# Kernel tuning notes

Hardware: AMD Instinct MI355X
Metric: run time of the kernel (lower is better)

The kernel has to match this reference:

```python
import jax, jax.numpy as jnp
import numpy as np

DN = ('NCDHW', 'OIDHW', 'NCDHW')  # torch Conv3d layout

def conv3d(x, w, b, pad):
    y = jax.lax.conv_general_dilated(x, w, (1, 1, 1), [(p, p) for p in pad], dimension_numbers=DN)
    return y + b[None, :, None, None, None]

def setup_inputs() -> dict:
    key = jax.random.key(0)
    ks = jax.random.split(key, 10)
    C, Cq = 64, 8  # in_channels, in_channels // 8
    s = 0.05
    x = jax.random.normal(ks[0], (2, C, 16, 16, 16), dtype=jnp.float32)
    return {
        'x': x,
        'wq': jax.random.normal(ks[1], (Cq, C, 1, 3, 1), jnp.float32) * s,
        'bq': jax.random.normal(ks[2], (Cq,), jnp.float32) * s,
        'wk': jax.random.normal(ks[3], (Cq, C, 3, 1, 1), jnp.float32) * s,
        'bk': jax.random.normal(ks[4], (Cq,), jnp.float32) * s,
        'wj': jax.random.normal(ks[5], (Cq, C, 1, 1, 3), jnp.float32) * s,
        'bj': jax.random.normal(ks[6], (Cq,), jnp.float32) * s,
        'wv': jax.random.normal(ks[7], (C, C, 1, 1, 1), jnp.float32) * s,
        'bv': jax.random.normal(ks[8], (C,), jnp.float32) * s,
        'gamma': jax.random.normal(ks[9], (1,), jnp.float32) * s,
    }

def reference(x, wq, bq, wk, bk, wj, bj, wv, bv, gamma):
    B, C, H, W, D = x.shape
    N = H * W * D
    q = conv3d(x, wq, bq, (0, 1, 0)).reshape(B, -1, N)   # [B, c, N]
    k = conv3d(x, wk, bk, (1, 0, 0)).reshape(B, -1, N)   # [B, c, N]
    j = conv3d(x, wj, bj, (0, 0, 1)).reshape(B, -1, N)   # [B, c, N]
    # affinity = (Q^T K) (J^T K) reassociated as Q^T (K J^T) K  -- identical math,
    # O(N^2 c) instead of O(N^3) since c = C//8 << N.
    kj = jnp.einsum('bcn,bdn->bcd', k, j)                # [B, c, c] = K @ J^T
    aff = jnp.einsum('bcn,bcd,bdm->bnm', q, kj, k)       # [B, N, N]
    aff = jax.nn.softmax(aff, axis=-1)
    v = conv3d(x, wv, bv, (0, 0, 0)).reshape(B, C, N)    # [B, C, N]
    weights = jnp.einsum('bcn,bnm->bcm', v, aff).reshape(B, C, H, W, D)
    return gamma * weights + x
```

## Files before the change

### kernel.cpp

```cpp
#include <hip/hip_runtime.h>

#define N 4096
#define CIN 64
#define NB 2

typedef unsigned short u16;
typedef short bf16x8 __attribute__((ext_vector_type(8)));
typedef float f32x4 __attribute__((ext_vector_type(4)));

#define OFF_QT 0
#define OFF_KT (OFF_QT + NB*N*8)
#define OFF_JT (OFF_KT + NB*N*8)
#define OFF_V  (OFF_JT + NB*N*8)
#define OFF_QK (OFF_V + NB*CIN*N)
#define OFF_MX (OFF_QK + NB*N*8)
#define OFF_SC (OFF_MX + NB*N)

__device__ __forceinline__ u16 f2bf(float f) {
    union { float f; unsigned u; } v; v.f = f;
    unsigned r = (v.u + 0x7fffu + ((v.u >> 16) & 1u)) >> 16;
    return (u16)r;
}

__global__ __launch_bounds__(512, 4) void prep(
        const float* __restrict__ x,
        const float* __restrict__ wq, const float* __restrict__ bq,
        const float* __restrict__ wk, const float* __restrict__ bk,
        const float* __restrict__ wj, const float* __restrict__ bj,
        const float* __restrict__ wv, const float* __restrict__ bv,
        float* __restrict__ ws, u16* __restrict__ vbf, float* __restrict__ out) {
    __shared__ union {
        float qkj[3][256];
        float accv[256][8];
    } sh;
    const int t    = threadIdx.x;
    const int tn   = t & 255;
    const int half = t >> 8;
    const int y    = blockIdx.y;
    const int b    = blockIdx.z;
    const int n    = blockIdx.x * 256 + tn;
    const float* xb = x + (size_t)b * CIN * N + n;
    const int c0base = half * 32;

    if (y < 8) {
        int cq = y;
        int d = n & 15, w = (n >> 4) & 15, h = n >> 8;
        int owl = (w > 0) ? -16 : 0,  owh = (w < 15) ? 16 : 0;
        int ohl = (h > 0) ? -256 : 0, ohh = (h < 15) ? 256 : 0;
        int odl = (d > 0) ? -1 : 0,   odh = (d < 15) ? 1 : 0;
        float mwl = (w > 0) ? 1.f : 0.f, mwh = (w < 15) ? 1.f : 0.f;
        float mhl = (h > 0) ? 1.f : 0.f, mhh = (h < 15) ? 1.f : 0.f;
        float mdl = (d > 0) ? 1.f : 0.f, mdh = (d < 15) ? 1.f : 0.f;
        float q = half ? 0.f : bq[cq];
        float k = half ? 0.f : bk[cq];
        float j = half ? 0.f : bj[cq];
        for (int c0i = 0; c0i < 32; c0i += 8) {
            const int c0 = c0base + c0i;
            float xc[8], xwl[8], xwh[8], xhl[8], xhh[8], xdl[8], xdh[8];
#pragma unroll
            for (int u = 0; u < 8; ++u) {
                const float* p = xb + (size_t)(c0 + u) * N;
                xc[u]  = p[0];
                xwl[u] = p[owl]; xwh[u] = p[owh];
                xhl[u] = p[ohl]; xhh[u] = p[ohh];
                xdl[u] = p[odl]; xdh[u] = p[odh];
            }
#pragma unroll
            for (int u = 0; u < 8; ++u) {
                int c = c0 + u;
                const float* wqr = wq + (cq * CIN + c) * 3;
                const float* wkr = wk + (cq * CIN + c) * 3;
                const float* wjr = wj + (cq * CIN + c) * 3;
                q += wqr[0] * (xwl[u] * mwl) + wqr[1] * xc[u] + wqr[2] * (xwh[u] * mwh);
                k += wkr[0] * (xhl[u] * mhl) + wkr[1] * xc[u] + wkr[2] * (xhh[u] * mhh);
                j += wjr[0] * (xdl[u] * mdl) + wjr[1] * xc[u] + wjr[2] * (xdh[u] * mdh);
            }
        }
        if (half) { sh.qkj[0][tn] = q; sh.qkj[1][tn] = k; sh.qkj[2][tn] = j; }
        __syncthreads();
        if (!half) {
            q += sh.qkj[0][tn]; k += sh.qkj[1][tn]; j += sh.qkj[2][tn];
            size_t base = (size_t)(b * N + n) * 8 + cq;
            ws[OFF_QT + base] = q;
            ws[OFF_KT + base] = k;
            ws[OFF_JT + base] = j;
        }
    } else {
        int yy = y - 8;
        int co0 = yy * 8;
        float acc[8];
#pragma unroll
        for (int i = 0; i < 8; ++i) acc[i] = half ? 0.f : bv[co0 + i];
        for (int c0i = 0; c0i < 32; c0i += 8) {
            const int c0 = c0base + c0i;
            float xv[8];
#pragma unroll
            for (int u = 0; u < 8; ++u) xv[u] = xb[(size_t)(c0 + u) * N];
#pragma unroll
            for (int u = 0; u < 8; ++u)
#pragma unroll
                for (int i = 0; i < 8; ++i)
                    acc[i] += wv[(co0 + i) * CIN + c0 + u] * xv[u];
            if ((c0 >> 3) == yy) {
#pragma unroll
                for (int u = 0; u < 8; ++u)
                    out[(size_t)(b * CIN + c0 + u) * N + n] = xv[u];
            }
        }
        if (half) {
#pragma unroll
            for (int i = 0; i < 8; ++i) sh.accv[tn][i] = acc[i];
        }
        __syncthreads();
        if (!half) {
#pragma unroll
            for (int i = 0; i < 8; ++i)
                vbf[(size_t)(b * CIN + co0 + i) * N + n] = f2bf(acc[i] + sh.accv[tn][i]);
        }
    }
}

__global__ __launch_bounds__(256) void kjqkj(const float* __restrict__ ws_in,
                                             float* __restrict__ ws) {
    __shared__ float kjpart[4][64];
    __shared__ float kjs[64];
    const int t = threadIdx.x, lane = t & 63, wid = t >> 6;
    const int b = blockIdx.y;
    const float* ktb = ws_in + OFF_KT + (size_t)b * N * 8;
    const float* jtb = ws_in + OFF_JT + (size_t)b * N * 8;
    const float* qtb = ws_in + OFF_QT + (size_t)b * N * 8;

    float acc[64];
#pragma unroll
    for (int i = 0; i < 64; ++i) acc[i] = 0.f;
    for (int i = 0; i < 16; ++i) {
        int nn = i * 256 + t;
        const float4* kt = (const float4*)(ktb + (size_t)nn * 8);
        const float4* jt = (const float4*)(jtb + (size_t)nn * 8);
        float4 ka = kt[0], kb = kt[1], ja = jt[0], jb = jt[1];
        float kv[8] = {ka.x, ka.y, ka.z, ka.w, kb.x, kb.y, kb.z, kb.w};
        float jv[8] = {ja.x, ja.y, ja.z, ja.w, jb.x, jb.y, jb.z, jb.w};
#pragma unroll
        for (int c = 0; c < 8; ++c)
#pragma unroll
            for (int dd = 0; dd < 8; ++dd) acc[c * 8 + dd] += kv[c] * jv[dd];
    }
#pragma unroll
    for (int s = 32; s >= 1; s >>= 1)
#pragma unroll
        for (int i = 0; i < 64; ++i) acc[i] += __shfl_down(acc[i], s, 64);
    if (lane == 0) {
#pragma unroll
        for (int i = 0; i < 64; ++i) kjpart[wid][i] = acc[i];
    }
    __syncthreads();
    if (t < 64) kjs[t] = kjpart[0][t] + kjpart[1][t] + kjpart[2][t] + kjpart[3][t];
    __syncthreads();

    float kjr[64];
#pragma unroll
    for (int i = 0; i < 64; ++i) kjr[i] = kjs[i];
    int m = blockIdx.x * 256 + t;
    const float4* qt = (const float4*)(qtb + (size_t)m * 8);
    float4 qa = qt[0], qb = qt[1];
    float qv[8] = {qa.x, qa.y, qa.z, qa.w, qb.x, qb.y, qb.z, qb.w};
    float o[8];
#pragma unroll
    for (int dd = 0; dd < 8; ++dd) {
        float a = 0.f;
#pragma unroll
        for (int c = 0; c < 8; ++c) a += qv[c] * kjr[c * 8 + dd];
        o[dd] = a;
    }
    float4* dst = (float4*)(ws + OFF_QK + (size_t)(b * N + m) * 8);
    dst[0] = make_float4(o[0], o[1], o[2], o[3]);
    dst[1] = make_float4(o[4], o[5], o[6], o[7]);
}

__global__ __launch_bounds__(512, 4) void pass1(const float* __restrict__ ws,
                                                float* __restrict__ mx_o, float* __restrict__ sc_o,
                                                const float* __restrict__ gamma) {
    __shared__ float smx[8][4];
    __shared__ float ssum[8][4];
    const int t = threadIdx.x, lane = t & 63, wid = t >> 6;
    const int r0 = blockIdx.x * 4;
    const int b  = r0 >> 12;
    const float* ktb = ws + OFF_KT + (size_t)b * N * 8;

    float4 qa[4], qb[4];
#pragma unroll
    for (int rr = 0; rr < 4; ++rr) {
        const float4* q4 = (const float4*)(ws + OFF_QK + (size_t)(r0 + rr) * 8);
        qa[rr] = q4[0]; qb[rr] = q4[1];
    }

    float as[4][8];
#pragma unroll
    for (int i = 0; i < 8; ++i) {
        const int m = wid * 512 + i * 64 + lane;
        const float4* kk4 = (const float4*)(ktb + (size_t)m * 8);
        float4 ka = kk4[0], kb2 = kk4[1];
#pragma unroll
        for (int rr = 0; rr < 4; ++rr)
            as[rr][i] = qa[rr].x * ka.x + qa[rr].y * ka.y + qa[rr].z * ka.z + qa[rr].w * ka.w
                      + qb[rr].x * kb2.x + qb[rr].y * kb2.y + qb[rr].z * kb2.z + qb[rr].w * kb2.w;
    }

    float mx[4];
#pragma unroll
    for (int rr = 0; rr < 4; ++rr) {
        float m01 = fmaxf(fmaxf(as[rr][0], as[rr][1]), fmaxf(as[rr][2], as[rr][3]));
        float m23 = fmaxf(fmaxf(as[rr][4], as[rr][5]), fmaxf(as[rr][6], as[rr][7]));
        mx[rr] = fmaxf(m01, m23);
    }
#pragma unroll
    for (int s = 32; s >= 1; s >>= 1)
#pragma unroll
        for (int rr = 0; rr < 4; ++rr)
            mx[rr] = fmaxf(mx[rr], __shfl_xor(mx[rr], s, 64));
    if (lane == 0) {
#pragma unroll
        for (int rr = 0; rr < 4; ++rr) smx[wid][rr] = mx[rr];
    }
    __syncthreads();
    float gm[4];
#pragma unroll
    for (int rr = 0; rr < 4; ++rr) {
        float g0 = fmaxf(fmaxf(smx[0][rr], smx[1][rr]), fmaxf(smx[2][rr], smx[3][rr]));
        float g1 = fmaxf(fmaxf(smx[4][rr], smx[5][rr]), fmaxf(smx[6][rr], smx[7][rr]));
        gm[rr] = fmaxf(g0, g1);
    }

    float sm[4];
#pragma unroll
    for (int rr = 0; rr < 4; ++rr) {
        float s0 = __expf(as[rr][0] - gm[rr]) + __expf(as[rr][1] - gm[rr])
                 + __expf(as[rr][2] - gm[rr]) + __expf(as[rr][3] - gm[rr]);
        float s1 = __expf(as[rr][4] - gm[rr]) + __expf(as[rr][5] - gm[rr])
                 + __expf(as[rr][6] - gm[rr]) + __expf(as[rr][7] - gm[rr]);
        sm[rr] = s0 + s1;
    }
#pragma unroll
    for (int s = 32; s >= 1; s >>= 1)
#pragma unroll
        for (int rr = 0; rr < 4; ++rr)
            sm[rr] += __shfl_xor(sm[rr], s, 64);
    if (lane == 0) {
#pragma unroll
        for (int rr = 0; rr < 4; ++rr) ssum[wid][rr] = sm[rr];
    }
    __syncthreads();
    if (t < 4) {
        float g0 = fmaxf(fmaxf(smx[0][t], smx[1][t]), fmaxf(smx[2][t], smx[3][t]));
        float g1 = fmaxf(fmaxf(smx[4][t], smx[5][t]), fmaxf(smx[6][t], smx[7][t]));
        float g  = fmaxf(g0, g1);
        float tt = ((ssum[0][t] + ssum[1][t]) + (ssum[2][t] + ssum[3][t]))
                 + ((ssum[4][t] + ssum[5][t]) + (ssum[6][t] + ssum[7][t]));
        mx_o[r0 + t] = g;
        sc_o[r0 + t] = gamma[0] / tt;
    }
}

__global__ __launch_bounds__(256) void pass2(const float* __restrict__ ws,
                                             const u16* __restrict__ vbf,
                                             float* __restrict__ out) {
    __shared__ u16 Pt[64][72];
    __shared__ u16 Vt[64][72];
    __shared__ float ks[64][8];
    const int t  = threadIdx.x;
    const int b  = blockIdx.z;
    const int m0 = blockIdx.x * 64;
    const int ns = blockIdx.y;
    const float* qkT = ws + OFF_QK + (size_t)b * N * 8;
    const float* ktb = ws + OFF_KT + (size_t)b * N * 8;
    const float* mxv = ws + OFF_MX + (size_t)b * N;
    const float* scv = ws + OFF_SC + (size_t)b * N;
    const u16*   vb  = vbf + (size_t)b * CIN * N;

    if (t < 128) ((float4*)ks)[t] = ((const float4*)(ktb + (size_t)m0 * 8))[t];

    const int lane = t & 63;
    const int wid  = t >> 6;
    const int l16  = lane & 15;
    const int lq   = lane >> 4;
    const int vc   = t >> 3;
    const int vseg = t & 7;

    f32x4 acc[4];
#pragma unroll
    for (int i = 0; i < 4; ++i) acc[i] = (f32x4){0.f, 0.f, 0.f, 0.f};

    for (int ch = 0; ch < 8; ++ch) {
        const int n0 = ns * 512 + ch * 64;
        const int n  = n0 + lane;
        const float4* q4 = (const float4*)(qkT + (size_t)n * 8);
        float4 qa = q4[0], qb = q4[1];
        float mxl = mxv[n], sl = scv[n];
        uint4 v0 = *(const uint4*)(vb + (size_t)vc        * N + n0 + vseg * 8);
        uint4 v1 = *(const uint4*)(vb + (size_t)(vc + 32) * N + n0 + vseg * 8);
        __syncthreads();
#pragma unroll
        for (int r = 0; r < 16; ++r) {
            int mi = wid * 16 + r;
            float4 k0 = *(const float4*)&ks[mi][0];
            float4 k1 = *(const float4*)&ks[mi][4];
            float a = qa.x * k0.x + qa.y * k0.y + qa.z * k0.z + qa.w * k0.w
                    + qb.x * k1.x + qb.y * k1.y + qb.z * k1.z + qb.w * k1.w;
            Pt[mi][lane] = f2bf(__expf(a - mxl) * sl);
        }
        *(uint4*)&Vt[vc][vseg * 8]      = v0;
        *(uint4*)&Vt[vc + 32][vseg * 8] = v1;
        __syncthreads();
#pragma unroll
        for (int kk = 0; kk < 2; ++kk) {
            int k0i = kk * 32 + lq * 8;
            bf16x8 bfrag = *(const bf16x8*)&Pt[wid * 16 + l16][k0i];
#pragma unroll
            for (int ct = 0; ct < 4; ++ct) {
                bf16x8 afrag = *(const bf16x8*)&Vt[ct * 16 + l16][k0i];
                acc[ct] = __builtin_amdgcn_mfma_f32_16x16x32_bf16(afrag, bfrag, acc[ct], 0, 0, 0);
            }
        }
    }
    float* ob = out + (size_t)b * CIN * N;
    const int mcol = m0 + wid * 16 + l16;
#pragma unroll
    for (int ct = 0; ct < 4; ++ct)
#pragma unroll
        for (int r = 0; r < 4; ++r) {
            int c = ct * 16 + lq * 4 + r;
            atomicAdd(&ob[(size_t)c * N + mcol], acc[ct][r]);
        }
}

extern "C" void kernel_launch(void* const* d_in, const int* in_sizes, int n_in,
                              void* d_out, int out_size, void* d_ws, size_t ws_size,
                              hipStream_t stream) {
    const float* x  = (const float*)d_in[0];
    const float* wq = (const float*)d_in[1];
    const float* bq = (const float*)d_in[2];
    const float* wk = (const float*)d_in[3];
    const float* bk = (const float*)d_in[4];
    const float* wj = (const float*)d_in[5];
    const float* bj = (const float*)d_in[6];
    const float* wv = (const float*)d_in[7];
    const float* bv = (const float*)d_in[8];
    const float* gamma = (const float*)d_in[9];
    float* ws  = (float*)d_ws;
    float* out = (float*)d_out;
    u16* vbf = (u16*)(ws + OFF_V);

    prep<<<dim3(16, 16, 2), 512, 0, stream>>>(x, wq, bq, wk, bk, wj, bj, wv, bv, ws, vbf, out);
    kjqkj<<<dim3(16, 2), 256, 0, stream>>>(ws, ws);
    pass1<<<2048, 512, 0, stream>>>(ws, ws + OFF_MX, ws + OFF_SC, gamma);
    pass2<<<dim3(64, 8, 2), 256, 0, stream>>>(ws, vbf, out);
}
```

Before: 155.7 us.

## Fuse KJ reduction into prep and Q·KJ projection into pass1, drop kjqkj kernel

Prep now computes all 8 q/k/j channels in one block per spatial tile instead of one block per channel, and emits partial K·J^T sums per tile into the workspace. Pass1 sums those 16 partials and forms Q·KJ on the fly, so the separate kjqkj launch and its serialized single-block-per-batch reduction are removed. The change also narrows pass2's LDS row padding from 72 to 68. The tradeoffs are higher register pressure in the fused qkj branch, redundant KJ summation in every pass1 block, and possible LDS bank conflicts from the new padding.

```diff
diff --git a/kernel.cpp b/kernel.cpp
--- a/kernel.cpp
+++ b/kernel.cpp
@@ -15,6 +15,7 @@
 #define OFF_QK (OFF_V + NB*CIN*N)
 #define OFF_MX (OFF_QK + NB*N*8)
 #define OFF_SC (OFF_MX + NB*N)
+#define OFF_KJ (OFF_SC + NB*N)
 
 __device__ __forceinline__ u16 f2bf(float f) {
     union { float f; unsigned u; } v; v.f = f;
@@ -30,20 +31,22 @@
         const float* __restrict__ wv, const float* __restrict__ bv,
         float* __restrict__ ws, u16* __restrict__ vbf, float* __restrict__ out) {
     __shared__ union {
-        float qkj[3][256];
+        float qkj[3][8][256];
         float accv[256][8];
     } sh;
+    __shared__ float kjpart[4][64];
     const int t    = threadIdx.x;
     const int tn   = t & 255;
     const int half = t >> 8;
     const int y    = blockIdx.y;
+    const int bx   = blockIdx.x;
     const int b    = blockIdx.z;
-    const int n    = blockIdx.x * 256 + tn;
+    const int n    = bx * 256 + tn;
     const float* xb = x + (size_t)b * CIN * N + n;
     const int c0base = half * 32;
 
-    if (y < 8) {
-        int cq = y;
+    if (y == 8) {
+        const int lane = t & 63, wid = t >> 6;
         int d = n & 15, w = (n >> 4) & 15, h = n >> 8;
         int owl = (w > 0) ? -16 : 0,  owh = (w < 15) ? 16 : 0;
         int ohl = (h > 0) ? -256 : 0, ohh = (h < 15) ? 256 : 0;
@@ -51,9 +54,13 @@
         float mwl = (w > 0) ? 1.f : 0.f, mwh = (w < 15) ? 1.f : 0.f;
         float mhl = (h > 0) ? 1.f : 0.f, mhh = (h < 15) ? 1.f : 0.f;
         float mdl = (d > 0) ? 1.f : 0.f, mdh = (d < 15) ? 1.f : 0.f;
-        float q = half ? 0.f : bq[cq];
-        float k = half ? 0.f : bk[cq];
-        float j = half ? 0.f : bj[cq];
+        float q[8], k[8], j[8];
+#pragma unroll
+        for (int cq = 0; cq < 8; ++cq) {
+            q[cq] = half ? 0.f : bq[cq];
+            k[cq] = half ? 0.f : bk[cq];
+            j[cq] = half ? 0.f : bj[cq];
+        }
         for (int c0i = 0; c0i < 32; c0i += 8) {
             const int c0 = c0base + c0i;
             float xc[8], xwl[8], xwh[8], xhl[8], xhh[8], xdl[8], xdh[8];
@@ -68,25 +75,69 @@
 #pragma unroll
             for (int u = 0; u < 8; ++u) {
                 int c = c0 + u;
-                const float* wqr = wq + (cq * CIN + c) * 3;
-                const float* wkr = wk + (cq * CIN + c) * 3;
-                const float* wjr = wj + (cq * CIN + c) * 3;
-                q += wqr[0] * (xwl[u] * mwl) + wqr[1] * xc[u] + wqr[2] * (xwh[u] * mwh);
-                k += wkr[0] * (xhl[u] * mhl) + wkr[1] * xc[u] + wkr[2] * (xhh[u] * mhh);
-                j += wjr[0] * (xdl[u] * mdl) + wjr[1] * xc[u] + wjr[2] * (xdh[u] * mdh);
-            }
-        }
-        if (half) { sh.qkj[0][tn] = q; sh.qkj[1][tn] = k; sh.qkj[2][tn] = j; }
+                float xwlm = xwl[u] * mwl, xwhm = xwh[u] * mwh;
+                float xhlm = xhl[u] * mhl, xhhm = xhh[u] * mhh;
+                float xdlm = xdl[u] * mdl, xdhm = xdh[u] * mdh;
+                float xcc  = xc[u];
+#pragma unroll
+                for (int cq = 0; cq < 8; ++cq) {
+                    const float* wqr = wq + (cq * CIN + c) * 3;
+                    const float* wkr = wk + (cq * CIN + c) * 3;
+                    const float* wjr = wj + (cq * CIN + c) * 3;
+                    q[cq] += wqr[0] * xwlm + wqr[1] * xcc + wqr[2] * xwhm;
+                    k[cq] += wkr[0] * xhlm + wkr[1] * xcc + wkr[2] * xhhm;
+                    j[cq] += wjr[0] * xdlm + wjr[1] * xcc + wjr[2] * xdhm;
+                }
+            }
+        }
+        if (half) {
+#pragma unroll
+            for (int cq = 0; cq < 8; ++cq) {
+                sh.qkj[0][cq][tn] = q[cq];
+                sh.qkj[1][cq][tn] = k[cq];
+                sh.qkj[2][cq][tn] = j[cq];
+            }
+        }
         __syncthreads();
         if (!half) {
-            q += sh.qkj[0][tn]; k += sh.qkj[1][tn]; j += sh.qkj[2][tn];
-            size_t base = (size_t)(b * N + n) * 8 + cq;
-            ws[OFF_QT + base] = q;
-            ws[OFF_KT + base] = k;
-            ws[OFF_JT + base] = j;
+#pragma unroll
+            for (int cq = 0; cq < 8; ++cq) {
+                q[cq] += sh.qkj[0][cq][tn];
+                k[cq] += sh.qkj[1][cq][tn];
+                j[cq] += sh.qkj[2][cq][tn];
+            }
+            size_t base = (size_t)(b * N + n) * 8;
+#pragma unroll
+            for (int cq = 0; cq < 8; ++cq) {
+                ws[OFF_QT + base + cq] = q[cq];
+                ws[OFF_KT + base + cq] = k[cq];
+                ws[OFF_JT + base + cq] = j[cq];
+            }
+#pragma unroll
+            for (int g = 0; g < 4; ++g) {
+                float a16[16];
+#pragma unroll
+                for (int cc = 0; cc < 2; ++cc)
+#pragma unroll
+                    for (int dd = 0; dd < 8; ++dd)
+                        a16[cc * 8 + dd] = k[g * 2 + cc] * j[dd];
+#pragma unroll
+                for (int s = 32; s >= 1; s >>= 1)
+#pragma unroll
+                    for (int i = 0; i < 16; ++i) a16[i] += __shfl_down(a16[i], s, 64);
+                if (lane == 0) {
+#pragma unroll
+                    for (int i = 0; i < 16; ++i) kjpart[wid][g * 16 + i] = a16[i];
+                }
+            }
+        }
+        __syncthreads();
+        if (t < 64) {
+            float s = kjpart[0][t] + kjpart[1][t] + kjpart[2][t] + kjpart[3][t];
+            ws[OFF_KJ + (size_t)(b * 16 + bx) * 64 + t] = s;
         }
     } else {
-        int yy = y - 8;
+        int yy = y;
         int co0 = yy * 8;
         float acc[8];
 #pragma unroll
@@ -120,78 +171,50 @@
     }
 }
 
-__global__ __launch_bounds__(256) void kjqkj(const float* __restrict__ ws_in,
-                                             float* __restrict__ ws) {
-    __shared__ float kjpart[4][64];
+__global__ __launch_bounds__(512, 4) void pass1(const float* __restrict__ ws_in,
+                                                float* __restrict__ ws,
+                                                const float* __restrict__ gamma) {
     __shared__ float kjs[64];
-    const int t = threadIdx.x, lane = t & 63, wid = t >> 6;
-    const int b = blockIdx.y;
-    const float* ktb = ws_in + OFF_KT + (size_t)b * N * 8;
-    const float* jtb = ws_in + OFF_JT + (size_t)b * N * 8;
-    const float* qtb = ws_in + OFF_QT + (size_t)b * N * 8;
-
-    float acc[64];
-#pragma unroll
-    for (int i = 0; i < 64; ++i) acc[i] = 0.f;
-    for (int i = 0; i < 16; ++i) {
-        int nn = i * 256 + t;
-        const float4* kt = (const float4*)(ktb + (size_t)nn * 8);
-        const float4* jt = (const float4*)(jtb + (size_t)nn * 8);
-        float4 ka = kt[0], kb = kt[1], ja = jt[0], jb = jt[1];
-        float kv[8] = {ka.x, ka.y, ka.z, ka.w, kb.x, kb.y, kb.z, kb.w};
-        float jv[8] = {ja.x, ja.y, ja.z, ja.w, jb.x, jb.y, jb.z, jb.w};
-#pragma unroll
-        for (int c = 0; c < 8; ++c)
-#pragma unroll
-            for (int dd = 0; dd < 8; ++dd) acc[c * 8 + dd] += kv[c] * jv[dd];
-    }
-#pragma unroll
-    for (int s = 32; s >= 1; s >>= 1)
-#pragma unroll
-        for (int i = 0; i < 64; ++i) acc[i] += __shfl_down(acc[i], s, 64);
-    if (lane == 0) {
-#pragma unroll
-        for (int i = 0; i < 64; ++i) kjpart[wid][i] = acc[i];
-    }
-    __syncthreads();
-    if (t < 64) kjs[t] = kjpart[0][t] + kjpart[1][t] + kjpart[2][t] + kjpart[3][t];
-    __syncthreads();
-
-    float kjr[64];
-#pragma unroll
-    for (int i = 0; i < 64; ++i) kjr[i] = kjs[i];
-    int m = blockIdx.x * 256 + t;
-    const float4* qt = (const float4*)(qtb + (size_t)m * 8);
-    float4 qa = qt[0], qb = qt[1];
-    float qv[8] = {qa.x, qa.y, qa.z, qa.w, qb.x, qb.y, qb.z, qb.w};
-    float o[8];
-#pragma unroll
-    for (int dd = 0; dd < 8; ++dd) {
-        float a = 0.f;
-#pragma unroll
-        for (int c = 0; c < 8; ++c) a += qv[c] * kjr[c * 8 + dd];
-        o[dd] = a;
-    }
-    float4* dst = (float4*)(ws + OFF_QK + (size_t)(b * N + m) * 8);
-    dst[0] = make_float4(o[0], o[1], o[2], o[3]);
-    dst[1] = make_float4(o[4], o[5], o[6], o[7]);
-}
-
-__global__ __launch_bounds__(512, 4) void pass1(const float* __restrict__ ws,
-                                                float* __restrict__ mx_o, float* __restrict__ sc_o,
-                                                const float* __restrict__ gamma) {
     __shared__ float smx[8][4];
     __shared__ float ssum[8][4];
     const int t = threadIdx.x, lane = t & 63, wid = t >> 6;
     const int r0 = blockIdx.x * 4;
     const int b  = r0 >> 12;
-    const float* ktb = ws + OFF_KT + (size_t)b * N * 8;
+    const float* ktb = ws_in + OFF_KT + (size_t)b * N * 8;
+
+    if (t < 64) {
+        const float* kjw = ws_in + OFF_KJ + (size_t)b * 16 * 64;
+        float s = 0.f;
+#pragma unroll
+        for (int p = 0; p < 16; ++p) s += kjw[p * 64 + t];
+        kjs[t] = s;
+    }
+    __syncthreads();
 
     float4 qa[4], qb[4];
 #pragma unroll
     for (int rr = 0; rr < 4; ++rr) {
-        const float4* q4 = (const float4*)(ws + OFF_QK + (size_t)(r0 + rr) * 8);
-        qa[rr] = q4[0]; qb[rr] = q4[1];
+        const float4* q4 = (const float4*)(ws_in + OFF_QT + (size_t)(r0 + rr) * 8);
+        float4 a4 = q4[0], b4 = q4[1];
+        float qv[8] = {a4.x, a4.y, a4.z, a4.w, b4.x, b4.y, b4.z, b4.w};
+        float o[8];
+#pragma unroll
+        for (int dd = 0; dd < 8; ++dd) {
+            float a = 0.f;
+#pragma unroll
+            for (int c = 0; c < 8; ++c) a += qv[c] * kjs[c * 8 + dd];
+            o[dd] = a;
+        }
+        qa[rr] = make_float4(o[0], o[1], o[2], o[3]);
+        qb[rr] = make_float4(o[4], o[5], o[6], o[7]);
+    }
+    if (wid == 0 && lane < 32) {
+        const int rr = lane >> 3, dd = lane & 7;
+        const float* qr = ws_in + OFF_QT + (size_t)(r0 + rr) * 8;
+        float o = 0.f;
+#pragma unroll
+        for (int c = 0; c < 8; ++c) o += qr[c] * kjs[c * 8 + dd];
+        ws[OFF_QK + (size_t)r0 * 8 + lane] = o;
     }
 
     float as[4][8];
@@ -256,16 +279,17 @@
         float g  = fmaxf(g0, g1);
         float tt = ((ssum[0][t] + ssum[1][t]) + (ssum[2][t] + ssum[3][t]))
                  + ((ssum[4][t] + ssum[5][t]) + (ssum[6][t] + ssum[7][t]));
-        mx_o[r0 + t] = g;
-        sc_o[r0 + t] = gamma[0] / tt;
-    }
-}
-
+        ws[OFF_MX + r0 + t] = g;
+        ws[OFF_SC + r0 + t] = gamma[0] / tt;
+    }
+}
+
+#define P2S 68
 __global__ __launch_bounds__(256) void pass2(const float* __restrict__ ws,
                                              const u16* __restrict__ vbf,
                                              float* __restrict__ out) {
-    __shared__ u16 Pt[64][72];
-    __shared__ u16 Vt[64][72];
+    __shared__ u16 Pt[64][P2S];
+    __shared__ u16 Vt[64][P2S];
     __shared__ float ks[64][8];
     const int t  = threadIdx.x;
     const int b  = blockIdx.z;
@@ -350,8 +374,7 @@
     float* out = (float*)d_out;
     u16* vbf = (u16*)(ws + OFF_V);
 
-    prep<<<dim3(16, 16, 2), 512, 0, stream>>>(x, wq, bq, wk, bk, wj, bj, wv, bv, ws, vbf, out);
-    kjqkj<<<dim3(16, 2), 256, 0, stream>>>(ws, ws);
-    pass1<<<2048, 512, 0, stream>>>(ws, ws + OFF_MX, ws + OFF_SC, gamma);
+    prep<<<dim3(16, 9, 2), 512, 0, stream>>>(x, wq, bq, wk, bk, wj, bj, wv, bv, ws, vbf, out);
+    pass1<<<2048, 512, 0, stream>>>(ws, ws, gamma);
     pass2<<<dim3(64, 8, 2), 256, 0, stream>>>(ws, vbf, out);
 }
```

Measured after the change: 428.5 us. 2.75x slower.
